# Kernel tuning notes

Measured on AMD Instinct MI355X. Metric: run time of the kernel, lower is better.

The kernel has to match this reference:

```python
import jax, jax.numpy as jnp
import numpy as np

TEMPERATURE = 2.0


def _offdiag_idx(n):
    # flat indices of the off-diagonal entries of an [n, n] matrix, row-major,
    # reshaped to [n, n-1] (matches torch masked_select(~eye).view(n, n-1))
    idx = np.arange(n * n).reshape(n, n)
    return jnp.asarray(idx[~np.eye(n, dtype=bool)].reshape(n, n - 1))


def setup_inputs() -> dict:
    key = jax.random.key(0)
    k1, k2, k3, k4 = jax.random.split(key, 4)
    B, D = 256, 512
    return {
        "wt_emb": jax.random.normal(k1, (B, D), dtype=jnp.float32),
        "mt_emb": jax.random.normal(k2, (B, D), dtype=jnp.float32),
        "label_wt": jax.random.uniform(k3, (B,), dtype=jnp.float32),
        "label_mt": jax.random.uniform(k4, (B,), dtype=jnp.float32),
    }


def reference(wt_emb, mt_emb, label_wt, label_mt):
    t = TEMPERATURE
    features = jnp.concatenate([wt_emb, mt_emb], axis=0)            # [n, D]
    labels = jnp.concatenate([label_wt, label_mt], axis=0)[:, None]  # [n, 1]
    n = features.shape[0]

    # L1 label differences: [n, n]
    label_diffs = jnp.abs(labels[:, None, :] - labels[None, :, :]).sum(-1)

    # negative L2 feature distances (safe sqrt: diagonal is exactly 0)
    diff = features[:, None, :] - features[None, :, :]               # [n, n, D]
    sq = jnp.sum(diff * diff, axis=-1)                               # [n, n]
    dist = jnp.where(sq > 0, jnp.sqrt(jnp.where(sq > 0, sq, 1.0)), 0.0)
    logits = -dist / t
    logits = logits - jax.lax.stop_gradient(jnp.max(logits, axis=1, keepdims=True))
    exp_logits = jnp.exp(logits)

    # drop diagonal -> [n, n-1]
    off = _offdiag_idx(n)
    lo = logits.reshape(-1)[off]
    eo = exp_logits.reshape(-1)[off]
    ldo = label_diffs.reshape(-1)[off]

    # vectorized over positive index k: mask[i, k, j] = ld[i, j] >= ld[i, k]
    neg_mask = ldo[:, None, :] >= ldo[:, :, None]                    # [n, n-1, n-1]
    denom = jnp.sum(jnp.where(neg_mask, eo[:, None, :], 0.0), axis=-1)  # [n, n-1]
    pos_log_probs = lo - jnp.log(denom)                              # [n, n-1]
    return -jnp.sum(pos_log_probs) / (n * (n - 1))
```

## Files before the change

### kernel.cpp

```cpp
#include <hip/hip_runtime.h>


#define N 512
#define B 256
#define D 512
#define NT 512
#define NBLK (N / 2)

#define WS_SL    0
#define WS_NORM  512
#define WS_PART  1024
#define WS_FH    2048
#define WS_G     (2048 + (N * D) / 2)

typedef _Float16 half4_t  __attribute__((ext_vector_type(4)));
typedef _Float16 half8_t  __attribute__((ext_vector_type(8)));
typedef float    f32x4    __attribute__((ext_vector_type(4)));

__global__ __launch_bounds__(NT) void sort_rows_kernel(
    const float* __restrict__ wt, const float* __restrict__ mt,
    const float* __restrict__ lwt, const float* __restrict__ lmt,
    float* __restrict__ ws)
{
    const int t = threadIdx.x, b = blockIdx.x;
    __shared__ float slab[N];
    __shared__ int scnt[32];
    slab[t] = (t < B) ? lwt[t] : lmt[t - B];
    if (t < 32) scnt[t] = 0;
    __syncthreads();

    const int jj = t & 31, j = b * 32 + jj, c = t >> 5;
    const float lj = slab[j];
    int r = 0;
    #pragma unroll 8
    for (int x = c * 32; x < c * 32 + 32; ++x) {
        const float v = slab[x];
        r += (v < lj || (v == lj && x < j)) ? 1 : 0;
    }
    atomicAdd(&scnt[jj], r);
    __syncthreads();

    if (t < 32)
        ws[WS_SL + scnt[t]] = slab[b * 32 + t];

    const int row = b * 32 + (t >> 4), s16 = t & 15;
    const int rr = scnt[t >> 4];
    const float* F = (row < B) ? (wt + (size_t)row * D) : (mt + (size_t)(row - B) * D);
    const float4* F4 = (const float4*)F;
    half4_t* Dst = (half4_t*)((_Float16*)(ws + WS_FH) + (size_t)rr * D);
    float nacc = 0.f;
    #pragma unroll
    for (int q = 0; q < 8; ++q) {
        const int idx = s16 + 16 * q;
        const float4 v = F4[idx];
        half4_t h;
        h[0] = (_Float16)v.x; h[1] = (_Float16)v.y;
        h[2] = (_Float16)v.z; h[3] = (_Float16)v.w;
        const float f0 = (float)h[0], f1 = (float)h[1];
        const float f2 = (float)h[2], f3 = (float)h[3];
        nacc += f0 * f0 + f1 * f1 + f2 * f2 + f3 * f3;
        Dst[idx] = h;
    }
    nacc += __shfl_down(nacc, 8, 16);
    nacc += __shfl_down(nacc, 4, 16);
    nacc += __shfl_down(nacc, 2, 16);
    nacc += __shfl_down(nacc, 1, 16);
    if (s16 == 0) ws[WS_NORM + rr] = nacc;
}

__global__ __launch_bounds__(256) void gram_kernel(float* __restrict__ ws)
{
    const int lane = threadIdx.x & 63;
    const int wid  = blockIdx.x * 4 + (threadIdx.x >> 6);
    const int ti = wid >> 5, tj = wid & 31;
    const int quad = lane >> 4, m = lane & 15;

    const _Float16* Fh = (const _Float16*)(ws + WS_FH);
    const _Float16* Arow = Fh + (size_t)(ti * 16 + m) * D + quad * 8;
    const _Float16* Brow = Fh + (size_t)(tj * 16 + m) * D + quad * 8;

    f32x4 acc = {0.f, 0.f, 0.f, 0.f};
    #pragma unroll
    for (int k0 = 0; k0 < D; k0 += 32) {
        const half8_t a = *(const half8_t*)(Arow + k0);
        const half8_t b = *(const half8_t*)(Brow + k0);
        acc = __builtin_amdgcn_mfma_f32_16x16x32_f16(a, b, acc, 0, 0, 0);
    }
    float* G = ws + WS_G;
    const int col = tj * 16 + m;
    #pragma unroll
    for (int rg = 0; rg < 4; ++rg)
        G[(size_t)(ti * 16 + quad * 4 + rg) * N + col] = acc[rg];
}

__global__ __launch_bounds__(NT) void rnc_main(float* __restrict__ ws)
{
    const int b = blockIdx.x, i0 = 2 * b, i1 = 2 * b + 1;
    const int t = threadIdx.x;
    const int w = t >> 6, lane = t & 63;

    __shared__ float sl[N];
    __shared__ float snm[N];
    __shared__ __align__(16) float sp0[N];
    __shared__ __align__(16) float sf0[N];
    __shared__ __align__(16) float sp1[N];
    __shared__ __align__(16) float sf1[N];
    __shared__ float sred[NT / 64];

    sl[t]  = ws[WS_SL + t];
    snm[t] = ws[WS_NORM + t];
    __syncthreads();
    const float li0 = sl[i0], li1 = sl[i1];
    const float ni0 = snm[i0], ni1 = snm[i1];

    const float* G = ws + WS_G;
    const float g0 = G[(size_t)i0 * N + t];
    const float g1 = G[(size_t)i1 * N + t];
    const float d0 = fmaxf(ni0 + snm[t] - 2.f * g0, 0.f);
    const float d1 = fmaxf(ni1 + snm[t] - 2.f * g1, 0.f);
    const float lg0 = -0.5f * sqrtf(d0);
    const float lg1 = -0.5f * sqrtf(d1);
    float lg_acc = 0.f;
    if (t != i0) lg_acc += lg0;
    if (t != i1) lg_acc += lg1;
    const float e0 = (t == i0) ? 0.f : __expf(lg0);
    const float e1 = (t == i1) ? 0.f : __expf(lg1);
    sp0[t] = e0; sf0[t] = e0;
    sp1[t] = e1; sf1[t] = e1;
    __syncthreads();

    if (w < 4) {
        float* arr = (w == 0) ? sp0 : (w == 1) ? sf0 : (w == 2) ? sp1 : sf1;
        float4* a4 = (float4*)arr;
        float4 u0 = a4[lane * 2], u1 = a4[lane * 2 + 1];
        float v0 = u0.x, v1 = u0.y, v2 = u0.z, v3 = u0.w;
        float v4 = u1.x, v5 = u1.y, v6 = u1.z, v7 = u1.w;
        if ((w & 1) == 0) {
            v1 += v0; v2 += v1; v3 += v2; v4 += v3; v5 += v4; v6 += v5; v7 += v6;
            float x = v7;
            #pragma unroll
            for (int off = 1; off < 64; off <<= 1) {
                const float y = __shfl_up(x, off, 64);
                if (lane >= off) x += y;
            }
            float ex = __shfl_up(x, 1, 64);
            if (lane == 0) ex = 0.f;
            v0 += ex; v1 += ex; v2 += ex; v3 += ex; v4 += ex; v5 += ex; v6 += ex; v7 += ex;
        } else {
            v6 += v7; v5 += v6; v4 += v5; v3 += v4; v2 += v3; v1 += v2; v0 += v1;
            float x = v0;
            #pragma unroll
            for (int off = 1; off < 64; off <<= 1) {
                const float y = __shfl_down(x, off, 64);
                if (lane + off < 64) x += y;
            }
            float ex = __shfl_down(x, 1, 64);
            if (lane == 63) ex = 0.f;
            v0 += ex; v1 += ex; v2 += ex; v3 += ex; v4 += ex; v5 += ex; v6 += ex; v7 += ex;
        }
        a4[lane * 2]     = make_float4(v0, v1, v2, v3);
        a4[lane * 2 + 1] = make_float4(v4, v5, v6, v7);
    }
    __syncthreads();

    float local = lg_acc;
    #pragma unroll
    for (int p = 0; p < 2; ++p) {
        const int x = t;
        const int ri = p ? i1 : i0;
        const float li = p ? li1 : li0;
        const float* SP = p ? sp1 : sp0;
        const float* SF = p ? sf1 : sf0;
        if (x != ri) {
            const float th = fabsf(li - sl[x]);
            int lo = 0, hi = ri + 1;
            while (lo < hi) {
                const int mid = (lo + hi) >> 1;
                if (fabsf(li - sl[mid]) >= th) lo = mid + 1; else hi = mid;
            }
            const int a = lo;
            lo = ri + 1; hi = N;
            while (lo < hi) {
                const int mid = (lo + hi) >> 1;
                if (fabsf(li - sl[mid]) >= th) hi = mid; else lo = mid + 1;
            }
            const int bb = lo;
            const float denom = ((a > 0) ? SP[a - 1] : 0.f) + ((bb < N) ? SF[bb] : 0.f);
            local -= __logf(denom);
        }
    }

    #pragma unroll
    for (int off = 32; off > 0; off >>= 1)
        local += __shfl_down(local, off, 64);
    if (lane == 0) sred[w] = local;
    __syncthreads();
    if (t == 0) {
        float sum = 0.f;
        #pragma unroll
        for (int k = 0; k < NT / 64; ++k) sum += sred[k];
        ws[WS_PART + b] = sum;
    }
}

__global__ __launch_bounds__(NBLK) void rnc_finalize(
    const float* __restrict__ ws, float* __restrict__ out)
{
    const int t = threadIdx.x;
    __shared__ float sred[NBLK / 64];
    float v = ws[WS_PART + t];
    #pragma unroll
    for (int off = 32; off > 0; off >>= 1)
        v += __shfl_down(v, off, 64);
    if ((t & 63) == 0) sred[t >> 6] = v;
    __syncthreads();
    if (t == 0) {
        float sum = 0.f;
        #pragma unroll
        for (int k = 0; k < NBLK / 64; ++k) sum += sred[k];
        out[0] = -sum / (float)((long)N * (N - 1));
    }
}

extern "C" void kernel_launch(void* const* d_in, const int* in_sizes, int n_in,
                              void* d_out, int out_size, void* d_ws, size_t ws_size,
                              hipStream_t stream) {
    const float* wt  = (const float*)d_in[0];
    const float* mt  = (const float*)d_in[1];
    const float* lwt = (const float*)d_in[2];
    const float* lmt = (const float*)d_in[3];
    float* out = (float*)d_out;
    float* ws  = (float*)d_ws;

    sort_rows_kernel<<<16, NT, 0, stream>>>(wt, mt, lwt, lmt, ws);
    gram_kernel<<<256, 256, 0, stream>>>(ws);
    rnc_main<<<NBLK, NT, 0, stream>>>(ws);
    rnc_finalize<<<1, NBLK, 0, stream>>>(ws, out);
}
```

Baseline: 75.26 us.

## Fuse Gram MFMA into main kernel and widen sort/convert grid

Removes the separate Gram-matrix kernel and its global N×N write/read. Each rnc_main block now computes its two rows of the Gram matrix with MFMA, keeping them in shared memory. The sort/convert kernel moves from 16 to 128 blocks, each handling 4 rows with wave-level reductions. This saves one launch and a global round trip, at the cost of redundant A-row loads and per-block MFMA work in which only 2 of the 16 A rows are useful.

New measurement: 83.37 us. +10.8%, slower.

```diff
diff --git a/kernel.cpp b/kernel.cpp
--- a/kernel.cpp
+++ b/kernel.cpp
@@ -11,7 +11,6 @@
 #define WS_NORM  512
 #define WS_PART  1024
 #define WS_FH    2048
-#define WS_G     (2048 + (N * D) / 2)
 
 typedef _Float16 half4_t  __attribute__((ext_vector_type(4)));
 typedef _Float16 half8_t  __attribute__((ext_vector_type(8)));
@@ -24,73 +23,47 @@
 {
     const int t = threadIdx.x, b = blockIdx.x;
     __shared__ float slab[N];
-    __shared__ int scnt[32];
+    __shared__ int scnt[4];
+    __shared__ float swred[NT / 64];
     slab[t] = (t < B) ? lwt[t] : lmt[t - B];
-    if (t < 32) scnt[t] = 0;
-    __syncthreads();
-
-    const int jj = t & 31, j = b * 32 + jj, c = t >> 5;
+    if (t < 4) scnt[t] = 0;
+    __syncthreads();
+
+    const int jj = t >> 7, j = b * 4 + jj;
+    const int c = t & 127;
     const float lj = slab[j];
     int r = 0;
-    #pragma unroll 8
-    for (int x = c * 32; x < c * 32 + 32; ++x) {
+    #pragma unroll
+    for (int x = c * 4; x < c * 4 + 4; ++x) {
         const float v = slab[x];
         r += (v < lj || (v == lj && x < j)) ? 1 : 0;
     }
-    atomicAdd(&scnt[jj], r);
-    __syncthreads();
-
-    if (t < 32)
-        ws[WS_SL + scnt[t]] = slab[b * 32 + t];
-
-    const int row = b * 32 + (t >> 4), s16 = t & 15;
-    const int rr = scnt[t >> 4];
-    const float* F = (row < B) ? (wt + (size_t)row * D) : (mt + (size_t)(row - B) * D);
-    const float4* F4 = (const float4*)F;
-    half4_t* Dst = (half4_t*)((_Float16*)(ws + WS_FH) + (size_t)rr * D);
-    float nacc = 0.f;
-    #pragma unroll
-    for (int q = 0; q < 8; ++q) {
-        const int idx = s16 + 16 * q;
-        const float4 v = F4[idx];
-        half4_t h;
-        h[0] = (_Float16)v.x; h[1] = (_Float16)v.y;
-        h[2] = (_Float16)v.z; h[3] = (_Float16)v.w;
-        const float f0 = (float)h[0], f1 = (float)h[1];
-        const float f2 = (float)h[2], f3 = (float)h[3];
-        nacc += f0 * f0 + f1 * f1 + f2 * f2 + f3 * f3;
-        Dst[idx] = h;
-    }
-    nacc += __shfl_down(nacc, 8, 16);
-    nacc += __shfl_down(nacc, 4, 16);
-    nacc += __shfl_down(nacc, 2, 16);
-    nacc += __shfl_down(nacc, 1, 16);
-    if (s16 == 0) ws[WS_NORM + rr] = nacc;
-}
-
-__global__ __launch_bounds__(256) void gram_kernel(float* __restrict__ ws)
-{
-    const int lane = threadIdx.x & 63;
-    const int wid  = blockIdx.x * 4 + (threadIdx.x >> 6);
-    const int ti = wid >> 5, tj = wid & 31;
-    const int quad = lane >> 4, m = lane & 15;
-
-    const _Float16* Fh = (const _Float16*)(ws + WS_FH);
-    const _Float16* Arow = Fh + (size_t)(ti * 16 + m) * D + quad * 8;
-    const _Float16* Brow = Fh + (size_t)(tj * 16 + m) * D + quad * 8;
-
-    f32x4 acc = {0.f, 0.f, 0.f, 0.f};
-    #pragma unroll
-    for (int k0 = 0; k0 < D; k0 += 32) {
-        const half8_t a = *(const half8_t*)(Arow + k0);
-        const half8_t b = *(const half8_t*)(Brow + k0);
-        acc = __builtin_amdgcn_mfma_f32_16x16x32_f16(a, b, acc, 0, 0, 0);
-    }
-    float* G = ws + WS_G;
-    const int col = tj * 16 + m;
-    #pragma unroll
-    for (int rg = 0; rg < 4; ++rg)
-        G[(size_t)(ti * 16 + quad * 4 + rg) * N + col] = acc[rg];
+    #pragma unroll
+    for (int off = 32; off > 0; off >>= 1)
+        r += __shfl_down(r, off, 64);
+    if ((t & 63) == 0) atomicAdd(&scnt[jj], r);
+    __syncthreads();
+
+    if (t < 4)
+        ws[WS_SL + scnt[t]] = slab[b * 4 + t];
+
+    const int rr = scnt[jj];
+    const float* F = (j < B) ? (wt + (size_t)j * D) : (mt + (size_t)(j - B) * D);
+    const float4 v = ((const float4*)F)[c];
+    half4_t h;
+    h[0] = (_Float16)v.x; h[1] = (_Float16)v.y;
+    h[2] = (_Float16)v.z; h[3] = (_Float16)v.w;
+    ((half4_t*)((_Float16*)(ws + WS_FH) + (size_t)rr * D))[c] = h;
+    const float f0 = (float)h[0], f1 = (float)h[1];
+    const float f2 = (float)h[2], f3 = (float)h[3];
+    float nacc = f0 * f0 + f1 * f1 + f2 * f2 + f3 * f3;
+    #pragma unroll
+    for (int off = 32; off > 0; off >>= 1)
+        nacc += __shfl_down(nacc, off, 64);
+    if ((t & 63) == 0) swred[t >> 6] = nacc;
+    __syncthreads();
+    if (t < 4)
+        ws[WS_NORM + scnt[t]] = swred[2 * t] + swred[2 * t + 1];
 }
 
 __global__ __launch_bounds__(NT) void rnc_main(float* __restrict__ ws)
@@ -105,17 +78,47 @@
     __shared__ __align__(16) float sf0[N];
     __shared__ __align__(16) float sp1[N];
     __shared__ __align__(16) float sf1[N];
+    __shared__ float sg0[N];
+    __shared__ float sg1[N];
     __shared__ float sred[NT / 64];
 
     sl[t]  = ws[WS_SL + t];
     snm[t] = ws[WS_NORM + t];
-    __syncthreads();
+
+    const _Float16* Fh = (const _Float16*)(ws + WS_FH);
+    const int quad = lane >> 4, m = lane & 15;
+    const _Float16* Ap = Fh + (size_t)(i0 + (m & 1)) * D + quad * 8;
+    const _Float16* Bp[4];
+    #pragma unroll
+    for (int u = 0; u < 4; ++u)
+        Bp[u] = Fh + (size_t)((w * 4 + u) * 16 + m) * D + quad * 8;
+
+    f32x4 acc[4] = {{0.f,0.f,0.f,0.f},{0.f,0.f,0.f,0.f},
+                    {0.f,0.f,0.f,0.f},{0.f,0.f,0.f,0.f}};
+    #pragma unroll
+    for (int k0 = 0; k0 < D; k0 += 32) {
+        const half8_t a = *(const half8_t*)(Ap + k0);
+        #pragma unroll
+        for (int u = 0; u < 4; ++u) {
+            const half8_t bb = *(const half8_t*)(Bp[u] + k0);
+            acc[u] = __builtin_amdgcn_mfma_f32_16x16x32_f16(a, bb, acc[u], 0, 0, 0);
+        }
+    }
+    if (quad == 0) {
+        #pragma unroll
+        for (int u = 0; u < 4; ++u) {
+            const int col = w * 64 + u * 16 + m;
+            sg0[col] = acc[u][0];
+            sg1[col] = acc[u][1];
+        }
+    }
+    __syncthreads();
+
     const float li0 = sl[i0], li1 = sl[i1];
     const float ni0 = snm[i0], ni1 = snm[i1];
 
-    const float* G = ws + WS_G;
-    const float g0 = G[(size_t)i0 * N + t];
-    const float g1 = G[(size_t)i1 * N + t];
+    const float g0 = sg0[t];
+    const float g1 = sg1[t];
     const float d0 = fmaxf(ni0 + snm[t] - 2.f * g0, 0.f);
     const float d1 = fmaxf(ni1 + snm[t] - 2.f * g1, 0.f);
     const float lg0 = -0.5f * sqrtf(d0);
@@ -232,8 +235,7 @@
     float* out = (float*)d_out;
     float* ws  = (float*)d_ws;
 
-    sort_rows_kernel<<<16, NT, 0, stream>>>(wt, mt, lwt, lmt, ws);
-    gram_kernel<<<256, 256, 0, stream>>>(ws);
+    sort_rows_kernel<<<128, NT, 0, stream>>>(wt, mt, lwt, lmt, ws);
     rnc_main<<<NBLK, NT, 0, stream>>>(ws);
     rnc_finalize<<<1, NBLK, 0, stream>>>(ws, out);
 }
```
